# Optimization experiments

Measured on AMD Instinct MI355X. Metric: run time of the kernel, lower is better.

Reference implementation:

```python
import jax, jax.numpy as jnp
import numpy as np

D_MODEL = 1024
NUM_HEADS = 16
D_K = D_MODEL // NUM_HEADS
ROPE_THETA = 10000.0


def _std(i, o):
    return (2.0 / (i + o)) ** 0.5


def setup_inputs() -> dict:
    key = jax.random.key(0)
    ks = jax.random.split(key, 5)
    B, S = 4, 2048
    x = jax.random.normal(ks[0], (B, S, D_MODEL), dtype=jnp.float32)
    s = _std(D_MODEL, D_MODEL)
    Wq = jax.random.normal(ks[1], (D_MODEL, D_MODEL), dtype=jnp.float32) * s
    Wk = jax.random.normal(ks[2], (D_MODEL, D_MODEL), dtype=jnp.float32) * s
    Wv = jax.random.normal(ks[3], (D_MODEL, D_MODEL), dtype=jnp.float32) * s
    Wo = jax.random.normal(ks[4], (D_MODEL, D_MODEL), dtype=jnp.float32) * s
    return {"x": x, "Wq": Wq, "Wk": Wk, "Wv": Wv, "Wo": Wo}


def _rope(t, cos, sin):
    # t: [b, h, s, d_k]; cos/sin: [s, d_k//2] broadcast over b, h
    te, to = t[..., ::2], t[..., 1::2]
    oe = te * cos - to * sin
    oo = te * sin + to * cos
    return jnp.stack([oe, oo], axis=-1).reshape(t.shape)  # interleave back


def reference(x, Wq, Wk, Wv, Wo):
    B, S, D = x.shape
    H, dk = NUM_HEADS, D_K

    def proj(W):
        y = jnp.einsum('bsi,oi->bso', x, W)
        return y.reshape(B, S, H, dk).transpose(0, 2, 1, 3)  # b h s d

    q, k, v = proj(Wq), proj(Wk), proj(Wv)

    # RoPE tables
    half = dk // 2
    inv_freq = 1.0 / (ROPE_THETA ** (jnp.arange(half, dtype=jnp.float32) / half))
    pos = jnp.arange(S, dtype=jnp.float32)
    freqs = pos[:, None] * inv_freq[None, :]  # [S, half]
    cos, sin = jnp.cos(freqs), jnp.sin(freqs)
    q = _rope(q, cos, sin)
    k = _rope(k, cos, sin)

    scale = 1.0 / (dk ** 0.5)
    scores = jnp.einsum('bhqd,bhkd->bhqk', q, k) * scale
    causal = jnp.tril(jnp.ones((S, S), dtype=bool))
    scores = jnp.where(causal[None, None], scores, -jnp.inf)
    probs = jax.nn.softmax(scores, axis=-1)
    out = jnp.einsum('bhqk,bhkd->bhqd', probs, v)
    out = out.transpose(0, 2, 1, 3).reshape(B, S, D)  # b s (h d)
    return jnp.einsum('bsi,oi->bso', out, Wo)
```

## Files before the change

### kernel.cpp

```cpp
#include <hip/hip_runtime.h>

#define DM 1024
#define NH 16
#define DK 64
#define NB 4
#define SEQ 2048
#define MTOT (NB*SEQ)

#ifndef __has_builtin
#define __has_builtin(x) 0
#endif

typedef __bf16 bf16x8 __attribute__((ext_vector_type(8)));
typedef float f32x4 __attribute__((ext_vector_type(4)));
typedef unsigned short u16x8 __attribute__((ext_vector_type(8)));
typedef unsigned int u32x4 __attribute__((ext_vector_type(4)));

static __device__ __forceinline__ float bf2f(unsigned int bits) {
  return __uint_as_float(bits << 16);
}
static __device__ __forceinline__ unsigned short f2bf(float x) {
  unsigned int u = __float_as_uint(x);
  return (unsigned short)((u + 0x7fffu + ((u >> 16) & 1u)) >> 16);
}
static __device__ __forceinline__ float fast_exp2(float x) {
#if __has_builtin(__builtin_amdgcn_exp2f)
  return __builtin_amdgcn_exp2f(x);
#else
  return exp2f(x);
#endif
}

#define CVTPK(d, a, b) \
  asm("v_cvt_pk_bf16_f32 %0, %1, %2" : "=v"(d) : "v"(a), "v"(b))

#define GLD16(gp, lp) __builtin_amdgcn_global_load_lds( \
    (const __attribute__((address_space(1))) void*)(gp), \
    (__attribute__((address_space(3))) void*)(lp), 16, 0, 0)

#define MFMA16(a, b, c) __builtin_amdgcn_mfma_f32_16x16x32_bf16((a), (b), (c), 0, 0, 0)

#define QSCALE 0.18033688011112042f
#define PSHIFT 23.083120654223414f

__global__ void prep_kernel(const float* __restrict__ x,
                            const float* __restrict__ Wq, const float* __restrict__ Wk,
                            const float* __restrict__ Wv, const float* __restrict__ Wo,
                            unsigned short* __restrict__ xb,
                            unsigned short* __restrict__ Wqkv,
                            unsigned short* __restrict__ Wob,
                            float2* __restrict__ tab) {
  const int bid = blockIdx.x, tid = threadIdx.x;
  if (bid < 4096) {
    int i = bid * 256 + tid;
    const float4* ip = reinterpret_cast<const float4*>(x) + (size_t)2 * i;
    float4 a = ip[0], b = ip[1];
    u16x8 o;
    o[0] = f2bf(a.x); o[1] = f2bf(a.y); o[2] = f2bf(a.z); o[3] = f2bf(a.w);
    o[4] = f2bf(b.x); o[5] = f2bf(b.y); o[6] = f2bf(b.z); o[7] = f2bf(b.w);
    reinterpret_cast<u16x8*>(xb)[i] = o;
  } else if (bid < 6144) {
    int j = (bid - 4096) * 256 + tid;
    int widx = j >> 17, i = j & 131071;
    const float* src; unsigned short* dst; float sc = 1.0f;
    switch (widx) {
      case 0:  src = Wq; dst = Wqkv; sc = QSCALE; break;
      case 1:  src = Wk; dst = Wqkv + (size_t)DM * DM; break;
      case 2:  src = Wv; dst = Wqkv + (size_t)2 * DM * DM; break;
      default: src = Wo; dst = Wob; break;
    }
    const float4* ip = reinterpret_cast<const float4*>(src) + (size_t)2 * i;
    float4 a = ip[0], b = ip[1];
    u16x8 o;
    o[0] = f2bf(a.x * sc); o[1] = f2bf(a.y * sc); o[2] = f2bf(a.z * sc); o[3] = f2bf(a.w * sc);
    o[4] = f2bf(b.x * sc); o[5] = f2bf(b.y * sc); o[6] = f2bf(b.z * sc); o[7] = f2bf(b.w * sc);
    reinterpret_cast<u16x8*>(dst)[i] = o;
  } else {
    int i = (bid - 6144) * 256 + tid;
    int s = i >> 5, f = i & 31;
    const float l2t_over_half = 0.415241011860920285f;
    float invf = exp2f(-(float)f * l2t_over_half);
    float fr = (float)s * invf;
    float sn, cs;
    sincosf(fr, &sn, &cs);
    tab[i] = make_float2(cs, sn);
  }
}

template <int MODE>
__global__ __launch_bounds__(256, 2) void gemm_bt_kernel(
    const unsigned short* __restrict__ A,
    const unsigned short* __restrict__ Bw,
    float* __restrict__ C,
    unsigned short* __restrict__ Qo,
    unsigned short* __restrict__ Ko,
    unsigned short* __restrict__ Vt,
    const float2* __restrict__ tab,
    int M, int N, int K) {
  __shared__ __align__(16) unsigned short As[2][128 * 64];
  __shared__ __align__(16) unsigned short Bs[2][128 * 64];
  const int t = threadIdx.x;
  const int l = t & 63;
  const int wm = (t >> 6) >> 1, wn = (t >> 6) & 1;
  const int lg = l >> 4, lc = l & 15;
  const int rx = lc & 7;

  const unsigned int nx = gridDim.x;
  unsigned int wg = blockIdx.y * nx + blockIdx.x;
  const unsigned int chunk = (nx * gridDim.y) >> 3;
  wg = (wg & 7) * chunk + (wg >> 3);
  const int bm = (wg / nx) * 128;
  const int bn = (wg % nx) * 128;

  f32x4 acc[4][4] = {};

  const int srow = t >> 3;
  const int schk = (t & 7) ^ (srow & 7);
  const unsigned short* ag = A + (size_t)(bm + srow) * K + schk * 8;
  const unsigned short* bg = Bw + (size_t)(bn + srow) * K + schk * 8;

#define GSTAGE(buf, k0) do {                                                  \
    GLD16(ag + (k0),                       As[buf] + t * 8);                  \
    GLD16(ag + (size_t)32 * K + (k0),      As[buf] + t * 8 + 2048);           \
    GLD16(ag + (size_t)64 * K + (k0),      As[buf] + t * 8 + 4096);           \
    GLD16(ag + (size_t)96 * K + (k0),      As[buf] + t * 8 + 6144);           \
    GLD16(bg + (k0),                       Bs[buf] + t * 8);                  \
    GLD16(bg + (size_t)32 * K + (k0),      Bs[buf] + t * 8 + 2048);           \
    GLD16(bg + (size_t)64 * K + (k0),      Bs[buf] + t * 8 + 4096);           \
    GLD16(bg + (size_t)96 * K + (k0),      Bs[buf] + t * 8 + 6144);           \
  } while (0)

  const int nt = K >> 6;
  GSTAGE(0, 0);

  for (int s = 0; s < nt; ++s) {
    const int cb = s & 1;
    if (s + 1 < nt) {
      GSTAGE(cb ^ 1, (s + 1) * 64);
      asm volatile("s_waitcnt vmcnt(8)" ::: "memory");
    } else {
      asm volatile("s_waitcnt vmcnt(0)" ::: "memory");
    }
    __builtin_amdgcn_s_barrier();

    bf16x8 af[2][4], bfr[2][4];
#pragma unroll
    for (int kk = 0; kk < 2; ++kk)
#pragma unroll
      for (int i = 0; i < 4; ++i) {
        const int ck = (((kk << 2) | lg) ^ rx) << 3;
        af[kk][i] = *reinterpret_cast<const bf16x8*>(
            &As[cb][(wm * 64 + i * 16 + lc) * 64 + ck]);
        bfr[kk][i] = *reinterpret_cast<const bf16x8*>(
            &Bs[cb][(wn * 64 + i * 16 + lc) * 64 + ck]);
      }
    __builtin_amdgcn_s_setprio(1);
#pragma unroll
    for (int kk = 0; kk < 2; ++kk)
#pragma unroll
      for (int i = 0; i < 4; ++i)
#pragma unroll
        for (int j = 0; j < 4; ++j)
          acc[i][j] = MFMA16(af[kk][i], bfr[kk][j], acc[i][j]);
    __builtin_amdgcn_s_setprio(0);
    asm volatile("s_waitcnt lgkmcnt(0)" ::: "memory");
    __builtin_amdgcn_s_barrier();
  }
#undef GSTAGE

  if (MODE == 1) {
#pragma unroll
    for (int i = 0; i < 4; ++i) {
#pragma unroll
      for (int j = 0; j < 4; ++j) {
        int n = bn + wn * 64 + j * 16 + lc;
#pragma unroll
        for (int r = 0; r < 4; ++r) {
          int m = bm + wm * 64 + i * 16 + lg * 4 + r;
          C[(size_t)m * N + n] = acc[i][j][r];
        }
      }
    }
  } else if (bn < 2 * DM) {
    const bool isQ = (bn < DM);
    unsigned short* dst = isQ ? Qo : Ko;
    const bool odd = (lc & 1) != 0;
#pragma unroll
    for (int i = 0; i < 4; ++i) {
#pragma unroll
      for (int j = 0; j < 4; ++j) {
        int n = bn + wn * 64 + j * 16 + lc;
        int nn = isQ ? n : n - DM;
        int h_ = nn >> 6, d_ = nn & 63;
        int f = d_ >> 1;
#pragma unroll
        for (int r = 0; r < 4; ++r) {
          int m = bm + wm * 64 + i * 16 + lg * 4 + r;
          int b_ = m >> 11, s_ = m & (SEQ - 1);
          float v = acc[i][j][r];
          float pv = __shfl_xor(v, 1);
          float2 cs = tab[(s_ << 5) | f];
          float res = odd ? fmaf(pv, cs.y, v * cs.x)
                          : fmaf(-pv, cs.y, v * cs.x);
          dst[(((size_t)b_ * NH + h_) * SEQ + s_) * DK + d_] = f2bf(res);
        }
      }
    }
  } else {
#pragma unroll
    for (int i = 0; i < 4; ++i) {
#pragma unroll
      for (int j = 0; j < 4; ++j) {
        int n = bn + wn * 64 + j * 16 + lc;
        int nn = n - 2 * DM, h_ = nn >> 6, d_ = nn & 63;
#pragma unroll
        for (int r = 0; r < 4; ++r) {
          int m = bm + wm * 64 + i * 16 + lg * 4 + r;
          int b_ = m >> 11, s_ = m & (SEQ - 1);
          Vt[(((size_t)b_ * NH + h_) * DK + d_) * SEQ + s_] = f2bf(acc[i][j][r]);
        }
      }
    }
  }
}

__global__ __launch_bounds__(256, 4) void attn_kernel(
    const unsigned short* __restrict__ Q,
    const unsigned short* __restrict__ Kc,
    const unsigned short* __restrict__ Vt,
    unsigned short* __restrict__ AO) {
  __shared__ __align__(16) unsigned short KL[2 * 4096];
  __shared__ __align__(16) unsigned short VL[2 * 4096];
  const int bh = blockIdx.x;
  const int y = (int)blockIdx.y;
  const int qt = (y < 4) ? 15 - y : (y < 8) ? 4 + y : (y < 12) ? y - 4 : 15 - y;
  const int t = threadIdx.x, w = t >> 6, l = t & 63, lg = l >> 4, lc = l & 15;
  const int b = bh >> 4, h = bh & 15;
  const int qrow0 = qt * 128 + w * 32;
  const int kendw = qrow0 + 32;
  const int nt = 2 * (qt + 1);
  const bool oddhi = (lg & 1) != 0;
  const int sig = ((lg & 1) << 1) | (lg >> 1);
  const int kx = lc & 7;

  const unsigned short* Qb = Q + (size_t)bh * SEQ * DK;
  const unsigned short* Kb = Kc + (size_t)bh * SEQ * DK;
  const unsigned short* Vb = Vt + (size_t)bh * DK * SEQ;

  const int srow = t >> 3;
  const int schk = (t & 7) ^ (srow & 7);
  const unsigned short* KsrcB = Kb + (size_t)srow * DK + (schk << 3);
  const unsigned short* VsrcB = Vb + (size_t)srow * SEQ + (schk << 3);

#define STAGE(buf, kbn) do {                                                   \
    GLD16(KsrcB + (size_t)(kbn) * DK,        KL + (buf) * 4096 + t * 8);       \
    GLD16(KsrcB + (size_t)((kbn) + 32) * DK, KL + (buf) * 4096 + 2048 + t * 8);\
    GLD16(VsrcB + (kbn),                     VL + (buf) * 4096 + t * 8);       \
    GLD16(VsrcB + (size_t)32 * SEQ + (kbn),  VL + (buf) * 4096 + 2048 + t * 8);\
  } while (0)

  bf16x8 aq[2][2];
#pragma unroll
  for (int i = 0; i < 2; ++i)
#pragma unroll
    for (int hk = 0; hk < 2; ++hk)
      aq[i][hk] = *reinterpret_cast<const bf16x8*>(
          Qb + (size_t)(qrow0 + i * 16 + lc) * DK + hk * 32 + lg * 8);

  f32x4 oacc[2][4] = {};
  f32x4 lacc[2] = {};
  bf16x8 ones;
#pragma unroll
  for (int j = 0; j < 8; ++j) ones[j] = (__bf16)1.0f;

  STAGE(0, 0);
  asm volatile("s_waitcnt vmcnt(0)" ::: "memory");
  __syncthreads();
  int cur = 0;

  for (int tile = 0; tile < nt; ++tile) {
    const int kb = tile * 64;
    if (tile + 1 < nt) STAGE(cur ^ 1, kb + 64);
    const unsigned short* KT = KL + cur * 4096;
    const unsigned short* VT = VL + cur * 4096;

#pragma unroll
    for (int h2 = 0; h2 < 2; ++h2) {
      const int hb = kb + h2 * 32;
      if (hb < kendw) {
        const int r0 = (h2 * 2) * 16 + lc, r1 = r0 + 16;
        bf16x8 kf0a = *reinterpret_cast<const bf16x8*>(KT + r0 * 64 + (((lg) ^ kx) << 3));
        bf16x8 kf0b = *reinterpret_cast<const bf16x8*>(KT + r0 * 64 + (((4 + lg) ^ kx) << 3));
        bf16x8 kf1a = *reinterpret_cast<const bf16x8*>(KT + r1 * 64 + (((lg) ^ kx) << 3));
        bf16x8 kf1b = *reinterpret_cast<const bf16x8*>(KT + r1 * 64 + (((4 + lg) ^ kx) << 3));

        f32x4 st[2][2] = {};
        __builtin_amdgcn_s_setprio(1);
        st[0][0] = MFMA16(kf0a, aq[0][0], st[0][0]);
        st[0][0] = MFMA16(kf0b, aq[0][1], st[0][0]);
        st[1][0] = MFMA16(kf0a, aq[1][0], st[1][0]);
        st[1][0] = MFMA16(kf0b, aq[1][1], st[1][0]);
        st[0][1] = MFMA16(kf1a, aq[0][0], st[0][1]);
        st[0][1] = MFMA16(kf1b, aq[0][1], st[0][1]);
        st[1][1] = MFMA16(kf1a, aq[1][0], st[1][1]);
        st[1][1] = MFMA16(kf1b, aq[1][1], st[1][1]);
        __builtin_amdgcn_s_setprio(0);

        const int vchk = ((h2 * 4 + sig) ^ kx) << 3;
        bf16x8 bv0 = *reinterpret_cast<const bf16x8*>(VT + (lc) * 64 + vchk);
        bf16x8 bv1 = *reinterpret_cast<const bf16x8*>(VT + (16 + lc) * 64 + vchk);
        bf16x8 bv2 = *reinterpret_cast<const bf16x8*>(VT + (32 + lc) * 64 + vchk);
        bf16x8 bv3 = *reinterpret_cast<const bf16x8*>(VT + (48 + lc) * 64 + vchk);

        if (hb + 31 > qrow0) {
#pragma unroll
          for (int i = 0; i < 2; ++i)
#pragma unroll
            for (int kt2 = 0; kt2 < 2; ++kt2) {
              int kq = qrow0 + i * 16 + lc - (hb + kt2 * 16 + lg * 4);
#pragma unroll
              for (int r = 0; r < 4; ++r)
                if (r > kq) st[i][kt2][r] = -1e30f;
            }
        }

        bf16x8 pa[2];
#pragma unroll
        for (int i = 0; i < 2; ++i) {
          float e00 = fast_exp2(st[i][0][0] - PSHIFT);
          float e01 = fast_exp2(st[i][0][1] - PSHIFT);
          float e02 = fast_exp2(st[i][0][2] - PSHIFT);
          float e03 = fast_exp2(st[i][0][3] - PSHIFT);
          float e10 = fast_exp2(st[i][1][0] - PSHIFT);
          float e11 = fast_exp2(st[i][1][1] - PSHIFT);
          float e12 = fast_exp2(st[i][1][2] - PSHIFT);
          float e13 = fast_exp2(st[i][1][3] - PSHIFT);
          unsigned int cA0, cA1, cB0, cB1;
          CVTPK(cA0, e00, e01);
          CVTPK(cA1, e02, e03);
          CVTPK(cB0, e10, e11);
          CVTPK(cB1, e12, e13);
          unsigned int sel0 = oddhi ? cA0 : cB0;
          unsigned int sel1 = oddhi ? cA1 : cB1;
          unsigned int q0 = (unsigned int)__shfl_xor((int)sel0, 16);
          unsigned int q1 = (unsigned int)__shfl_xor((int)sel1, 16);
          u32x4 pu;
          pu[0] = oddhi ? q0 : cA0;
          pu[1] = oddhi ? q1 : cA1;
          pu[2] = oddhi ? cB0 : q0;
          pu[3] = oddhi ? cB1 : q1;
          pa[i] = __builtin_bit_cast(bf16x8, pu);
        }

        __builtin_amdgcn_s_setprio(1);
        lacc[0] = MFMA16(pa[0], ones, lacc[0]);
        lacc[1] = MFMA16(pa[1], ones, lacc[1]);
        oacc[0][0] = MFMA16(pa[0], bv0, oacc[0][0]);
        oacc[1][0] = MFMA16(pa[1], bv0, oacc[1][0]);
        oacc[0][1] = MFMA16(pa[0], bv1, oacc[0][1]);
        oacc[1][1] = MFMA16(pa[1], bv1, oacc[1][1]);
        oacc[0][2] = MFMA16(pa[0], bv2, oacc[0][2]);
        oacc[1][2] = MFMA16(pa[1], bv2, oacc[1][2]);
        oacc[0][3] = MFMA16(pa[0], bv3, oacc[0][3]);
        oacc[1][3] = MFMA16(pa[1], bv3, oacc[1][3]);
        __builtin_amdgcn_s_setprio(0);
      }
    }

    asm volatile("s_waitcnt vmcnt(0)" ::: "memory");
    __syncthreads();
    cur ^= 1;
  }
#undef STAGE

#pragma unroll
  for (int i = 0; i < 2; ++i)
#pragma unroll
    for (int r = 0; r < 4; ++r) {
      float inv = 1.0f / lacc[i][r];
      int qg = qrow0 + i * 16 + lg * 4 + r;
      unsigned short* ao = AO + ((size_t)b * SEQ + qg) * DM + h * DK;
#pragma unroll
      for (int d = 0; d < 4; ++d)
        ao[d * 16 + lc] = f2bf(oacc[i][d][r] * inv);
    }
}

extern "C" void kernel_launch(void* const* d_in, const int* in_sizes, int n_in,
                              void* d_out, int out_size, void* d_ws, size_t ws_size,
                              hipStream_t stream) {
  (void)in_sizes; (void)n_in; (void)out_size; (void)ws_size;
  const float* x  = (const float*)d_in[0];
  const float* Wq = (const float*)d_in[1];
  const float* Wk = (const float*)d_in[2];
  const float* Wv = (const float*)d_in[3];
  const float* Wo = (const float*)d_in[4];
  float* out = (float*)d_out;

  char* ws = (char*)d_ws;
  size_t off = 0;
  auto carve = [&](size_t bytes) -> void* {
    void* p = (void*)(ws + off);
    off += (bytes + 255) & ~(size_t)255;
    return p;
  };
  unsigned short* xb   = (unsigned short*)carve((size_t)MTOT * DM * 2);
  unsigned short* Wqkv = (unsigned short*)carve((size_t)3 * DM * DM * 2);
  unsigned short* Wob  = (unsigned short*)carve((size_t)DM * DM * 2);
  unsigned short* Qb   = (unsigned short*)carve((size_t)NB * NH * SEQ * DK * 2);
  unsigned short* Kb   = (unsigned short*)carve((size_t)NB * NH * SEQ * DK * 2);
  unsigned short* Vtb  = (unsigned short*)carve((size_t)NB * NH * SEQ * DK * 2);
  unsigned short* AOb  = (unsigned short*)carve((size_t)MTOT * DM * 2);
  float2* tab          = (float2*)carve((size_t)SEQ * 32 * sizeof(float2));

  prep_kernel<<<6400, 256, 0, stream>>>(x, Wq, Wk, Wv, Wo, xb, Wqkv, Wob, tab);

  gemm_bt_kernel<0><<<dim3(3 * DM / 128, MTOT / 128), 256, 0, stream>>>(
      xb, Wqkv, nullptr, Qb, Kb, Vtb, tab, MTOT, 3 * DM, DM);

  attn_kernel<<<dim3(NB * NH, 16), 256, 0, stream>>>(Qb, Kb, Vtb, AOb);

  gemm_bt_kernel<1><<<dim3(DM / 128, MTOT / 128), 256, 0, stream>>>(
      AOb, Wob, out, nullptr, nullptr, nullptr, nullptr, MTOT, DM, DM);
}
```

Measured before the change: 155.0 us.

## Stage Q/K RoPE epilogue through LDS for coalesced 16-byte stores; remap XCD tiles

The Q/K projection epilogue now writes the accumulator tile into shared memory with a swizzled layout, then each thread reads eight consecutive features, applies RoPE and stores them as one 16-byte bf16 vector per row. This replaces scattered 2-byte global stores and the cross-lane shuffles. The workgroup-to-tile mapping is also rewritten so each XCD takes a contiguous band of M tiles in 8x8 groups, aimed at better L2 reuse. The cost is two extra barriers and an LDS round trip. The new mapping hardcodes the grid shape.

```diff
diff --git a/kernel.cpp b/kernel.cpp
--- a/kernel.cpp
+++ b/kernel.cpp
@@ -87,6 +87,8 @@
   }
 }
 
+#define LWIDX(m, n) ((m) * 128 + ((((n) >> 3) ^ ((m) & 15)) << 3) + ((n) & 7))
+
 template <int MODE>
 __global__ __launch_bounds__(256, 2) void gemm_bt_kernel(
     const unsigned short* __restrict__ A,
@@ -97,20 +99,19 @@
     unsigned short* __restrict__ Vt,
     const float2* __restrict__ tab,
     int M, int N, int K) {
-  __shared__ __align__(16) unsigned short As[2][128 * 64];
-  __shared__ __align__(16) unsigned short Bs[2][128 * 64];
+  __shared__ __align__(16) unsigned short Sbuf[4][128 * 64];
   const int t = threadIdx.x;
   const int l = t & 63;
   const int wm = (t >> 6) >> 1, wn = (t >> 6) & 1;
   const int lg = l >> 4, lc = l & 15;
   const int rx = lc & 7;
 
-  const unsigned int nx = gridDim.x;
-  unsigned int wg = blockIdx.y * nx + blockIdx.x;
-  const unsigned int chunk = (nx * gridDim.y) >> 3;
-  wg = (wg & 7) * chunk + (wg >> 3);
-  const int bm = (wg / nx) * 128;
-  const int bn = (wg % nx) * 128;
+  const unsigned int wgl = blockIdx.y * gridDim.x + blockIdx.x;
+  const int xcd = wgl & 7;
+  const int idx = (int)(wgl >> 3);
+  const int sq = idx >> 6, r6 = idx & 63;
+  const int bm = (xcd * 8 + (r6 >> 3)) * 128;
+  const int bn = (sq * 8 + (r6 & 7)) * 128;
 
   f32x4 acc[4][4] = {};
 
@@ -120,14 +121,14 @@
   const unsigned short* bg = Bw + (size_t)(bn + srow) * K + schk * 8;
 
 #define GSTAGE(buf, k0) do {                                                  \
-    GLD16(ag + (k0),                       As[buf] + t * 8);                  \
-    GLD16(ag + (size_t)32 * K + (k0),      As[buf] + t * 8 + 2048);           \
-    GLD16(ag + (size_t)64 * K + (k0),      As[buf] + t * 8 + 4096);           \
-    GLD16(ag + (size_t)96 * K + (k0),      As[buf] + t * 8 + 6144);           \
-    GLD16(bg + (k0),                       Bs[buf] + t * 8);                  \
-    GLD16(bg + (size_t)32 * K + (k0),      Bs[buf] + t * 8 + 2048);           \
-    GLD16(bg + (size_t)64 * K + (k0),      Bs[buf] + t * 8 + 4096);           \
-    GLD16(bg + (size_t)96 * K + (k0),      Bs[buf] + t * 8 + 6144);           \
+    GLD16(ag + (k0),                  &Sbuf[buf][t * 8]);                     \
+    GLD16(ag + (size_t)32 * K + (k0), &Sbuf[buf][t * 8 + 2048]);              \
+    GLD16(ag + (size_t)64 * K + (k0), &Sbuf[buf][t * 8 + 4096]);              \
+    GLD16(ag + (size_t)96 * K + (k0), &Sbuf[buf][t * 8 + 6144]);              \
+    GLD16(bg + (k0),                  &Sbuf[2 + (buf)][t * 8]);               \
+    GLD16(bg + (size_t)32 * K + (k0), &Sbuf[2 + (buf)][t * 8 + 2048]);        \
+    GLD16(bg + (size_t)64 * K + (k0), &Sbuf[2 + (buf)][t * 8 + 4096]);        \
+    GLD16(bg + (size_t)96 * K + (k0), &Sbuf[2 + (buf)][t * 8 + 6144]);        \
   } while (0)
 
   const int nt = K >> 6;
@@ -150,9 +151,9 @@
       for (int i = 0; i < 4; ++i) {
         const int ck = (((kk << 2) | lg) ^ rx) << 3;
         af[kk][i] = *reinterpret_cast<const bf16x8*>(
-            &As[cb][(wm * 64 + i * 16 + lc) * 64 + ck]);
+            &Sbuf[cb][(wm * 64 + i * 16 + lc) * 64 + ck]);
         bfr[kk][i] = *reinterpret_cast<const bf16x8*>(
-            &Bs[cb][(wn * 64 + i * 16 + lc) * 64 + ck]);
+            &Sbuf[2 + cb][(wn * 64 + i * 16 + lc) * 64 + ck]);
       }
     __builtin_amdgcn_s_setprio(1);
 #pragma unroll
@@ -184,27 +185,40 @@
   } else if (bn < 2 * DM) {
     const bool isQ = (bn < DM);
     unsigned short* dst = isQ ? Qo : Ko;
-    const bool odd = (lc & 1) != 0;
-#pragma unroll
-    for (int i = 0; i < 4; ++i) {
+    const int nnb = isQ ? bn : bn - DM;
+    float* L = reinterpret_cast<float*>(&Sbuf[0][0]);
+    __syncthreads();
+#pragma unroll
+    for (int i = 0; i < 4; ++i)
 #pragma unroll
       for (int j = 0; j < 4; ++j) {
-        int n = bn + wn * 64 + j * 16 + lc;
-        int nn = isQ ? n : n - DM;
-        int h_ = nn >> 6, d_ = nn & 63;
-        int f = d_ >> 1;
-#pragma unroll
-        for (int r = 0; r < 4; ++r) {
-          int m = bm + wm * 64 + i * 16 + lg * 4 + r;
-          int b_ = m >> 11, s_ = m & (SEQ - 1);
-          float v = acc[i][j][r];
-          float pv = __shfl_xor(v, 1);
-          float2 cs = tab[(s_ << 5) | f];
-          float res = odd ? fmaf(pv, cs.y, v * cs.x)
-                          : fmaf(-pv, cs.y, v * cs.x);
-          dst[(((size_t)b_ * NH + h_) * SEQ + s_) * DK + d_] = f2bf(res);
-        }
-      }
+        const int ml = wm * 64 + i * 16 + lg * 4;
+        const int nl = wn * 64 + j * 16 + lc;
+#pragma unroll
+        for (int r = 0; r < 4; ++r)
+          L[LWIDX(ml + r, nl)] = acc[i][j][r];
+      }
+    __syncthreads();
+    const int b_ = bm >> 11;
+    const int s_base = bm & (SEQ - 1);
+    const int w4 = t >> 6;
+    const int c = l & 15;
+    const int h_ = (nnb >> 6) + (c >> 3);
+    unsigned short* db = dst + (((size_t)b_ * NH + h_) * SEQ) * DK + (c & 7) * 8;
+#pragma unroll
+    for (int it = 0; it < 8; ++it) {
+      const int m = w4 * 32 + it * 4 + (l >> 4);
+      const float* Lp = L + (m * 128 + ((c ^ (m & 15)) << 3));
+      const int s_g = s_base + m;
+      u16x8 o;
+#pragma unroll
+      for (int f4 = 0; f4 < 4; ++f4) {
+        float v0 = Lp[2 * f4], v1 = Lp[2 * f4 + 1];
+        float2 cs = tab[(s_g << 5) | ((c & 7) * 4 + f4)];
+        o[2 * f4]     = f2bf(fmaf(-v1, cs.y, v0 * cs.x));
+        o[2 * f4 + 1] = f2bf(fmaf(v0, cs.y, v1 * cs.x));
+      }
+      *reinterpret_cast<u16x8*>(db + (size_t)s_g * DK) = o;
     }
   } else {
 #pragma unroll
```

Result: faster. 141.0 us (median of 2 runs) (-9.0%).
